# Performance work log

Measured on AMD Instinct MI355X. Metric: run time of the kernel, lower is better.

Reference implementation:

```python
import jax, jax.numpy as jnp
import numpy as np

T = 8192          # sequence length
D = 1024          # input_size
H = 16            # n_heads
HEAD = 64         # head_size = hidden_size // n_heads


def setup_inputs() -> dict:
    key = jax.random.key(0)
    ks = jax.random.split(key, 8)
    lim = (1.0 / HEAD) ** 0.5
    u = lambda k, shape: jax.random.uniform(k, shape, minval=-lim, maxval=lim, dtype=jnp.float32)
    return {
        "xs": jax.random.normal(ks[0], (T, D), dtype=jnp.float32),
        "if_weights": u(ks[1], (H, 2, D)),
        "o_weights": u(ks[2], (H, HEAD, D)),
        "kq_weights": u(ks[3], (H, 2 * HEAD, D)),
        "v_weights": u(ks[4], (H, HEAD, D)),
        "if_bias": u(ks[5], (H, 2)),
        "o_bias": u(ks[6], (H, HEAD)),
        "kvq_bias": u(ks[7], (H, 3, HEAD)),
    }


def reference(xs, if_weights, o_weights, kq_weights, v_weights, if_bias, o_bias, kvq_bias):
    inv_sqrt_head = 1.0 / jnp.sqrt(jnp.asarray(HEAD, jnp.float32))

    def step(state, x):
        h_prev, c_prev, m_prev, n_prev = state
        # gates
        i_f = jnp.einsum('htd,d->ht', if_weights, x) + if_bias          # (H, 2)
        o = jax.nn.sigmoid(jnp.einsum('hkd,d->hk', o_weights, x) + o_bias)  # (H, HEAD)
        i, f = i_f[:, 0], i_f[:, 1]
        # log-space stabilizer
        m = jnp.maximum(f + m_prev, i)
        i = jnp.exp(i - m)
        f = jnp.exp(f + m_prev - m)
        # key/query/value projections
        kq = jnp.einsum('hkd,d->hk', kq_weights, x)                      # (H, 2*HEAD)
        k, q = kq[:, :HEAD], kq[:, HEAD:]
        v = jnp.einsum('hkd,d->hk', v_weights, x)
        k = k * inv_sqrt_head + kvq_bias[:, 0]
        v = v + kvq_bias[:, 1]
        q = q + kvq_bias[:, 2]
        # state updates
        n = f[:, None] * n_prev + i[:, None] * k                          # (H, HEAD)
        c = f[:, None, None] * c_prev + i[:, None, None] * (v[:, :, None] * k[:, None, :])  # (H, HEAD, HEAD)
        # readout
        h = jnp.einsum('hij,hj->hi', c, q)                                # (H, HEAD)
        denom = jnp.maximum(jnp.abs(jnp.einsum('hj,hj->h', n, q)), 1.0)  # (H,)
        h = o * (h / denom[:, None])
        return (h, c, m, n), h.reshape(H * HEAD)

    init = (
        jnp.zeros((H, HEAD), jnp.float32),
        jnp.zeros((H, HEAD, HEAD), jnp.float32),
        jnp.zeros((H,), jnp.float32),
        jnp.zeros((H, HEAD), jnp.float32),
    )
    _, hs = jax.lax.scan(step, init, xs)
    return hs  # (T, hidden_size)
```

## Files before the change

### kernel.cpp

```cpp
#include <hip/hip_runtime.h>
#include <math.h>

#define T_LEN 8192
#define D_IN  1024
#define NH    16
#define NPAD  4224
#define NCH   128
#define NGRP  8
#define GSZ   16
#define NPACK 16896
#define NCONV 4096

typedef __attribute__((ext_vector_type(8))) _Float16 f16x8;
typedef __attribute__((ext_vector_type(4))) _Float16 f16x4;
typedef __attribute__((ext_vector_type(4))) float f32x4;

static const size_t OFF_WP   = 0;
static const size_t OFF_BG   = 2300000;
static const size_t OFF_BIAS = OFF_WP + (size_t)NPAD * D_IN;
static const size_t OFF_P    = OFF_BIAS + NPAD;
static const size_t OFF_M    = OFF_P + (size_t)T_LEN * NPAD;
static const size_t OFF_DC   = OFF_M + (size_t)T_LEN * NH;
static const size_t OFF_DN   = OFF_DC + (size_t)NCH * NH * 64 * 64;
static const size_t OFF_DL   = OFF_DN + (size_t)NCH * NH * 64;
static const size_t OFF_IF   = OFF_DL + (size_t)NCH * NH;

__device__ __forceinline__ void glds16(const void* g, void* l) {
  __builtin_amdgcn_global_load_lds(
      (const __attribute__((address_space(1))) void*)g,
      (__attribute__((address_space(3))) void*)l, 16, 0, 0);
}

__global__ __launch_bounds__(256) void pack_conv(
    const float* __restrict__ ifw, const float* __restrict__ ow,
    const float* __restrict__ kqw, const float* __restrict__ vw,
    const float* __restrict__ ifb, const float* __restrict__ ob,
    const float* __restrict__ kvqb, _Float16* __restrict__ Wph,
    float* __restrict__ bias,
    const float* __restrict__ X, _Float16* __restrict__ Xh) {
  int b = blockIdx.x;
  if (b < NPACK) {
    int idx = b * 256 + threadIdx.x;
    int n = idx >> 10, d = idx & 1023;
    float w = 0.f, bb = 0.f;
    if (n < 32) {
      int h = n >> 1, t = n & 1;
      w = ifw[(h * 2 + t) * D_IN + d];
      bb = ifb[h * 2 + t];
    } else if (n < 4128) {
      int r = n - 32;
      int h = r >> 8, j = r & 255;
      if (j < 64)       { w = kqw[(h * 128 + j) * D_IN + d] * 0.125f; bb = kvqb[(h * 3 + 0) * 64 + j]; }
      else if (j < 128) { w = kqw[(h * 128 + j) * D_IN + d];          bb = kvqb[(h * 3 + 2) * 64 + (j - 64)]; }
      else if (j < 192) { w = vw[(h * 64 + (j - 128)) * D_IN + d];    bb = kvqb[(h * 3 + 1) * 64 + (j - 128)]; }
      else              { w = ow[(h * 64 + (j - 192)) * D_IN + d];    bb = ob[h * 64 + (j - 192)]; }
    }
    Wph[(size_t)n * D_IN + d] = (_Float16)w;
    if (d == 0) bias[n] = bb;
  } else {
    int i = ((b - NPACK) * 256 + threadIdx.x) << 3;
    float4 v0 = *(const float4*)(X + i);
    float4 v1 = *(const float4*)(X + i + 4);
    f16x8 r;
    r[0] = (_Float16)v0.x; r[1] = (_Float16)v0.y; r[2] = (_Float16)v0.z; r[3] = (_Float16)v0.w;
    r[4] = (_Float16)v1.x; r[5] = (_Float16)v1.y; r[6] = (_Float16)v1.z; r[7] = (_Float16)v1.w;
    *(f16x8*)(Xh + i) = r;
  }
}

__global__ __launch_bounds__(256) void gemm_f16(
    const _Float16* __restrict__ Xh, const _Float16* __restrict__ Wph,
    const float* __restrict__ bias, _Float16* __restrict__ Ph) {
  __shared__ _Float16 As[2][128 * 32];
  __shared__ _Float16 Bs[2][128 * 32];
  int tid = threadIdx.x;
  int wave = tid >> 6, lane = tid & 63;
  int wgid = blockIdx.x;
  int virt = (wgid & 7) * 264 + (wgid >> 3);
  int mt = virt / 33, nt = virt % 33;
  int m0 = mt << 7, n0 = nt << 7;
  int wr = wave >> 1, wc = wave & 1;

  f32x4 acc[4][4];
  f32x4 zero = {0.f, 0.f, 0.f, 0.f};
#pragma unroll
  for (int i = 0; i < 4; ++i)
#pragma unroll
    for (int j = 0; j < 4; ++j) acc[i][j] = zero;

  int srow = lane >> 2;
  int scol = (((lane & 3) ^ ((lane >> 3) & 3)) << 3);
  const _Float16* ga = Xh + (size_t)(m0 + wave * 32 + srow) * D_IN + scol;
  const _Float16* gb = Wph + (size_t)(n0 + wave * 32 + srow) * D_IN + scol;
  int lds0 = (wave * 32) * 32;
  int lds1 = (wave * 32 + 16) * 32;

  int fr = lane & 15;
  int fko = (((lane >> 4) ^ ((fr >> 1) & 3)) << 3);

  glds16(ga, &As[0][lds0]);
  glds16(ga + 16 * D_IN, &As[0][lds1]);
  glds16(gb, &Bs[0][lds0]);
  glds16(gb + 16 * D_IN, &Bs[0][lds1]);
  __syncthreads();

  int cur = 0;
  for (int k0 = 0; k0 < D_IN; k0 += 32) {
    if (k0 + 32 < D_IN) {
      int kn = k0 + 32;
      glds16(ga + kn, &As[cur ^ 1][lds0]);
      glds16(ga + 16 * D_IN + kn, &As[cur ^ 1][lds1]);
      glds16(gb + kn, &Bs[cur ^ 1][lds0]);
      glds16(gb + 16 * D_IN + kn, &Bs[cur ^ 1][lds1]);
    }
    f16x8 a[4], b[4];
#pragma unroll
    for (int mi = 0; mi < 4; ++mi)
      a[mi] = *(const f16x8*)&As[cur][(wr * 64 + mi * 16 + fr) * 32 + fko];
#pragma unroll
    for (int ni = 0; ni < 4; ++ni)
      b[ni] = *(const f16x8*)&Bs[cur][(wc * 64 + ni * 16 + fr) * 32 + fko];
#pragma unroll
    for (int mi = 0; mi < 4; ++mi)
#pragma unroll
      for (int ni = 0; ni < 4; ++ni)
        acc[mi][ni] = __builtin_amdgcn_mfma_f32_16x16x32_f16(a[mi], b[ni], acc[mi][ni], 0, 0, 0);
    __syncthreads();
    cur ^= 1;
  }

  int cr = (lane >> 4) << 2;
  int cc = lane & 15;
#pragma unroll
  for (int mi = 0; mi < 4; ++mi) {
#pragma unroll
    for (int ni = 0; ni < 4; ++ni) {
      int col = n0 + wc * 64 + ni * 16 + cc;
      float bb = bias[col];
      size_t base = (size_t)(m0 + wr * 64 + mi * 16 + cr) * NPAD + col;
#pragma unroll
      for (int r = 0; r < 4; ++r)
        Ph[base + (size_t)r * NPAD] = (_Float16)(acc[mi][ni][r] + bb);
    }
  }
}

__global__ __launch_bounds__(256) void gemm_if(
    const float* __restrict__ X, const float* __restrict__ ifw,
    const float* __restrict__ ifb, float* __restrict__ IFc) {
  __shared__ float Xs[64 * 72];
  __shared__ float Ws[32 * 68];
  int tid = threadIdx.x;
  int r0 = blockIdx.x << 6;
  int nc = tid & 15;
  int rg = tid >> 4;
  int n0 = nc << 1;
  int sw = ((n0 >> 3) & 3) << 2;
  int sx = (rg & 3) << 2;

  float acc[4][2];
#pragma unroll
  for (int j = 0; j < 4; ++j) { acc[j][0] = 0.f; acc[j][1] = 0.f; }

  for (int k0 = 0; k0 < D_IN; k0 += 64) {
    __syncthreads();
#pragma unroll
    for (int i = 0; i < 4; ++i) {
      int fi = (i << 8) + tid;
      int row = fi >> 4, kk = (fi & 15) << 2;
      float4 v = *(const float4*)(X + (size_t)(r0 + row) * D_IN + k0 + kk);
      *(float4*)&Xs[row * 72 + (kk ^ (((row >> 2) & 3) << 2))] = v;
    }
#pragma unroll
    for (int i = 0; i < 2; ++i) {
      int fi = (i << 8) + tid;
      int row = fi >> 4, kk = (fi & 15) << 2;
      float4 v = *(const float4*)(ifw + (size_t)row * D_IN + k0 + kk);
      *(float4*)&Ws[row * 68 + (kk ^ (((row >> 3) & 3) << 2))] = v;
    }
    __syncthreads();
#pragma unroll
    for (int k4 = 0; k4 < 64; k4 += 4) {
      float4 w0 = *(const float4*)&Ws[n0 * 68 + (k4 ^ sw)];
      float4 w1 = *(const float4*)&Ws[(n0 + 1) * 68 + (k4 ^ sw)];
#pragma unroll
      for (int j = 0; j < 4; ++j) {
        float4 xv = *(const float4*)&Xs[((rg << 2) + j) * 72 + (k4 ^ sx)];
        acc[j][0] = fmaf(xv.x, w0.x, acc[j][0]);
        acc[j][0] = fmaf(xv.y, w0.y, acc[j][0]);
        acc[j][0] = fmaf(xv.z, w0.z, acc[j][0]);
        acc[j][0] = fmaf(xv.w, w0.w, acc[j][0]);
        acc[j][1] = fmaf(xv.x, w1.x, acc[j][1]);
        acc[j][1] = fmaf(xv.y, w1.y, acc[j][1]);
        acc[j][1] = fmaf(xv.z, w1.z, acc[j][1]);
        acc[j][1] = fmaf(xv.w, w1.w, acc[j][1]);
      }
    }
  }
  float b0 = ifb[n0], b1 = ifb[n0 + 1];
#pragma unroll
  for (int j = 0; j < 4; ++j) {
    int row = r0 + (rg << 2) + j;
    float2 st; st.x = acc[j][0] + b0; st.y = acc[j][1] + b1;
    *(float2*)(IFc + ((size_t)row << 5) + n0) = st;
  }
}

__global__ __launch_bounds__(256) void mscan(const float* __restrict__ IFc, float* __restrict__ M) {
  int h = blockIdx.x;
  int tid = threadIdx.x;
  int lane = tid & 63, wv = tid >> 6;
  int t0 = tid << 5;
  float F = 0.f, I = -1e30f;
#pragma unroll 8
  for (int u = 0; u < 32; ++u) {
    float2 v = *(const float2*)(IFc + ((size_t)(t0 + u) << 5) + (h << 1));
    I = fmaxf(I + v.y, v.x);
    F += v.y;
  }
#pragma unroll
  for (int d = 1; d < 64; d <<= 1) {
    float Fo = __shfl_up(F, d, 64);
    float Io = __shfl_up(I, d, 64);
    if (lane >= d) { I = fmaxf(Io + F, I); F = Fo + F; }
  }
  __shared__ float sF[4], sI[4];
  if (lane == 63) { sF[wv] = F; sI[wv] = I; }
  float Fe = __shfl_up(F, 1, 64);
  float Ie = __shfl_up(I, 1, 64);
  if (lane == 0) { Fe = 0.f; Ie = -1e30f; }
  __syncthreads();
  float Fp = 0.f, Ip = -1e30f;
  for (int w = 0; w < wv; ++w) { Ip = fmaxf(Ip + sF[w], sI[w]); Fp += sF[w]; }
  float Ft = Fp + Fe;
  float It = fmaxf(Ip + Fe, Ie);
  float m = fmaxf(Ft, It);
#pragma unroll 8
  for (int u = 0; u < 32; ++u) {
    float2 v = *(const float2*)(IFc + ((size_t)(t0 + u) << 5) + (h << 1));
    m = fmaxf(v.y + m, v.x);
    M[(size_t)(t0 + u) * NH + h] = m;
  }
}

__global__ __launch_bounds__(256) void d1_dc(
    const _Float16* __restrict__ Ph, const float* __restrict__ IFc,
    const float* __restrict__ M,
    _Float16* __restrict__ DCh, float* __restrict__ DN, float* __restrict__ DL) {
  int c = blockIdx.x >> 4, h = blockIdx.x & 15;
  int t0 = c << 6, hb = 32 + (h << 8);
  int tid = threadIdx.x;
  int lane = tid & 63, wave = tid >> 6;
  __shared__ _Float16 Kt[64 * 72];
  __shared__ _Float16 Vt[64 * 72];
  __shared__ float gl[64];
#pragma unroll
  for (int i = 0; i < 2; ++i) {
    int fq = (i << 8) + tid;
    int s = fq >> 3, b8 = (fq & 7) << 3;
    const _Float16* row = Ph + (size_t)(t0 + s) * NPAD + hb;
    f16x8 kv = *(const f16x8*)(row + b8);
    f16x8 vv = *(const f16x8*)(row + 128 + b8);
#pragma unroll
    for (int j = 0; j < 8; ++j) {
      Kt[(b8 + j) * 72 + s] = kv[j];
      Vt[(b8 + j) * 72 + s] = vv[j];
    }
  }
  if (tid < 64) {
    float2 iff = *(const float2*)(IFc + ((size_t)(t0 + tid) << 5) + (h << 1));
    float iv = iff.x, fv = iff.y;
    float cs = fv;
#pragma unroll
    for (int dd = 1; dd < 64; dd <<= 1) {
      float o = __shfl_up(cs, dd, 64);
      cs += (tid >= dd) ? o : 0.f;
    }
    float cumL = __shfl(cs, 63, 64);
    float mL = M[(size_t)(t0 + 63) * NH + h];
    gl[tid] = __expf(cumL - cs + iv - mL);
    if (tid == 0) {
      float mstart = (c > 0) ? M[(size_t)(t0 - 1) * NH + h] : 0.f;
      DL[(c << 4) + h] = __expf(mstart + cumL - mL);
    }
  }
  __syncthreads();
  if (tid < 64) {
    float acc = 0.f;
#pragma unroll
    for (int s = 0; s < 64; ++s) acc = fmaf(gl[s], (float)Kt[tid * 72 + s], acc);
    DN[((size_t)(c << 4) + h) * 64 + tid] = acc;
  }
  int arow = lane & 15;
  int kq = (lane >> 4) << 3;
  int aR = (wave << 4) + arow;
  f16x8 ag0, ag1;
#pragma unroll
  for (int j = 0; j < 8; ++j) {
    ag0[j] = (_Float16)(gl[kq + j] * (float)Vt[aR * 72 + kq + j]);
    ag1[j] = (_Float16)(gl[32 + kq + j] * (float)Vt[aR * 72 + 32 + kq + j]);
  }
  f32x4 accD[4];
  f32x4 zero = {0.f, 0.f, 0.f, 0.f};
#pragma unroll
  for (int n = 0; n < 4; ++n) accD[n] = zero;
#pragma unroll
  for (int n = 0; n < 4; ++n) {
    f16x8 b0 = *(const f16x8*)&Kt[((n << 4) + arow) * 72 + kq];
    f16x8 b1 = *(const f16x8*)&Kt[((n << 4) + arow) * 72 + 32 + kq];
    accD[n] = __builtin_amdgcn_mfma_f32_16x16x32_f16(ag0, b0, accD[n], 0, 0, 0);
    accD[n] = __builtin_amdgcn_mfma_f32_16x16x32_f16(ag1, b1, accD[n], 0, 0, 0);
  }
  __syncthreads();
  int crow = (lane >> 4) << 2, cc = lane & 15;
#pragma unroll
  for (int n = 0; n < 4; ++n)
#pragma unroll
    for (int r = 0; r < 4; ++r)
      Vt[((wave << 4) + crow + r) * 72 + (n << 4) + cc] = (_Float16)accD[n][r];
  __syncthreads();
  size_t base = ((size_t)(c << 4) + h) << 12;
#pragma unroll
  for (int i = 0; i < 2; ++i) {
    int fq = (i << 8) + tid;
    int a = fq >> 3, b8 = (fq & 7) << 3;
    *(f16x8*)(DCh + base + ((size_t)a << 6) + b8) = *(const f16x8*)&Vt[a * 72 + b8];
  }
}

__global__ __launch_bounds__(256) void d2a(
    const _Float16* __restrict__ DCh, const float* __restrict__ DN,
    const float* __restrict__ DL,
    float* __restrict__ BgDC, float* __restrict__ BgDN, float* __restrict__ Ag) {
  int bid = blockIdx.x, tid = threadIdx.x;
  if (bid < 2048) {
    int linear = (bid << 8) + tid;
    int g = linear >> 16, e = linear & 65535;
    int h = e >> 12;
    float carry = 0.f, a = 1.f;
    size_t idx = (size_t)e + ((size_t)g << 4) * 65536;
    float v = (float)DCh[idx];
    for (int u = 0; u < GSZ; ++u) {
      float dl = DL[(((g << 4) + u) << 4) + h];
      float vn = (u < GSZ - 1) ? (float)DCh[idx + 65536] : 0.f;
      carry = fmaf(dl, carry, v);
      a *= dl;
      v = vn;
      idx += 65536;
    }
    BgDC[((size_t)g << 16) + e] = carry;
    if ((e & 4095) == 0) Ag[(g << 4) + h] = a;
  } else {
    int linear = ((bid - 2048) << 8) + tid;
    int g = linear >> 10, e = linear & 1023;
    int h = e >> 6;
    float carry = 0.f;
    size_t idx = (size_t)e + ((size_t)g << 4) * 1024;
    float v = DN[idx];
    for (int u = 0; u < GSZ; ++u) {
      float dl = DL[(((g << 4) + u) << 4) + h];
      float vn = (u < GSZ - 1) ? DN[idx + 1024] : 0.f;
      carry = fmaf(dl, carry, v);
      v = vn;
      idx += 1024;
    }
    BgDN[(g << 10) + e] = carry;
  }
}

__global__ __launch_bounds__(256) void d2c(
    _Float16* __restrict__ DCh, float* __restrict__ DN,
    const float* __restrict__ DL,
    const float* __restrict__ BgDC, const float* __restrict__ BgDN,
    const float* __restrict__ Ag) {
  int bid = blockIdx.x, tid = threadIdx.x;
  if (bid < 2048) {
    int linear = (bid << 8) + tid;
    int g = linear >> 16, e = linear & 65535;
    int h = e >> 12;
    float P = 0.f;
    for (int gp = 0; gp < g; ++gp)
      P = fmaf(Ag[(gp << 4) + h], P, BgDC[((size_t)gp << 16) + e]);
    float carry = P;
    size_t idx = (size_t)e + ((size_t)g << 4) * 65536;
    float v = (float)DCh[idx];
    for (int u = 0; u < GSZ; ++u) {
      float dl = DL[(((g << 4) + u) << 4) + h];
      float vn = (u < GSZ - 1) ? (float)DCh[idx + 65536] : 0.f;
      DCh[idx] = (_Float16)carry;
      carry = fmaf(dl, carry, v);
      v = vn;
      idx += 65536;
    }
  } else {
    int linear = ((bid - 2048) << 8) + tid;
    int g = linear >> 10, e = linear & 1023;
    int h = e >> 6;
    float P = 0.f;
    for (int gp = 0; gp < g; ++gp)
      P = fmaf(Ag[(gp << 4) + h], P, BgDN[(gp << 10) + e]);
    float carry = P;
    size_t idx = (size_t)e + ((size_t)g << 4) * 1024;
    float v = DN[idx];
    for (int u = 0; u < GSZ; ++u) {
      float dl = DL[(((g << 4) + u) << 4) + h];
      float vn = (u < GSZ - 1) ? DN[idx + 1024] : 0.f;
      DN[idx] = carry;
      carry = fmaf(dl, carry, v);
      v = vn;
      idx += 1024;
    }
  }
}

__global__ __launch_bounds__(256) void d3_out(
    const _Float16* __restrict__ Ph, const float* __restrict__ IFc,
    const float* __restrict__ M,
    const _Float16* __restrict__ CS, const float* __restrict__ NS,
    float* __restrict__ out) {
  int c = blockIdx.x >> 4, h = blockIdx.x & 15;
  int t0 = c << 6, hb = 32 + (h << 8);
  int tid = threadIdx.x;
  int lane = tid & 63, wave = tid >> 6;
  __shared__ _Float16 Kh[64 * 72];
  __shared__ _Float16 Qh[64 * 72];
  __shared__ _Float16 Vt[64 * 72];
  __shared__ _Float16 Ch[64 * 72];
  __shared__ _Float16 Oh[64 * 72];
  __shared__ _Float16 Pl[64 * 72];
  __shared__ float cf[64], il[64], ml[64], dl[64], nq[64], nsl[64];

#pragma unroll
  for (int i = 0; i < 2; ++i) {
    int fq = (i << 8) + tid;
    int s = fq >> 3, b8 = (fq & 7) << 3;
    const _Float16* row = Ph + (size_t)(t0 + s) * NPAD + hb;
    f16x8 kv = *(const f16x8*)(row + b8);
    f16x8 qv = *(const f16x8*)(row + 64 + b8);
    f16x8 vv = *(const f16x8*)(row + 128 + b8);
    f16x8 ov = *(const f16x8*)(row + 192 + b8);
    f16x8 cv = *(const f16x8*)(CS + ((((size_t)(c << 4)) + h) << 12) + ((size_t)s << 6) + b8);
    *(f16x8*)&Kh[s * 72 + b8] = kv;
    *(f16x8*)&Qh[s * 72 + b8] = qv;
    *(f16x8*)&Oh[s * 72 + b8] = ov;
    *(f16x8*)&Ch[s * 72 + b8] = cv;
#pragma unroll
    for (int j = 0; j < 8; ++j) Vt[(b8 + j) * 72 + s] = vv[j];
  }
  __syncthreads();

  float iv = 0.f, mt = 0.f, cs = 0.f;
  if (tid < 64) {
    float2 iff = *(const float2*)(IFc + ((size_t)(t0 + tid) << 5) + (h << 1));
    iv = iff.x;
    float fv = iff.y;
    mt = M[(size_t)(t0 + tid) * NH + h];
    nsl[tid] = NS[((size_t)(c << 4) + h) * 64 + tid];
    cs = fv;
#pragma unroll
    for (int dd = 1; dd < 64; dd <<= 1) {
      float o = __shfl_up(cs, dd, 64);
      cs += (tid >= dd) ? o : 0.f;
    }
  }
  __syncthreads();
  if (tid < 64) {
    cf[tid] = cs; il[tid] = iv; ml[tid] = mt;
    float mstart = (c > 0) ? M[(size_t)(t0 - 1) * NH + h] : 0.f;
    dl[tid] = __expf(mstart + cs - mt);
    float acc = 0.f;
#pragma unroll
    for (int b = 0; b < 64; ++b) acc = fmaf(nsl[b], (float)Qh[tid * 72 + b], acc);
    nq[tid] = acc;
  }
  __syncthreads();

  int band = wave << 4;
  int arow = lane & 15;
  int kq = (lane >> 4) << 3;
  int crow = (lane >> 4) << 2;

  f16x8 aq0 = *(const f16x8*)&Qh[(band + arow) * 72 + kq];
  f16x8 aq1 = *(const f16x8*)&Qh[(band + arow) * 72 + 32 + kq];

  f32x4 S[4];
  f32x4 zero = {0.f, 0.f, 0.f, 0.f};
#pragma unroll
  for (int n = 0; n < 4; ++n) S[n] = zero;
#pragma unroll
  for (int n = 0; n < 4; ++n) {
    f16x8 b0 = *(const f16x8*)&Kh[((n << 4) + arow) * 72 + kq];
    f16x8 b1 = *(const f16x8*)&Kh[((n << 4) + arow) * 72 + 32 + kq];
    S[n] = __builtin_amdgcn_mfma_f32_16x16x32_f16(aq0, b0, S[n], 0, 0, 0);
    S[n] = __builtin_amdgcn_mfma_f32_16x16x32_f16(aq1, b1, S[n], 0, 0, 0);
  }

  float cft[4], mlt[4];
#pragma unroll
  for (int r = 0; r < 4; ++r) {
    int t = band + crow + r;
    cft[r] = cf[t]; mlt[r] = ml[t];
  }
  float rsum[4] = {0.f, 0.f, 0.f, 0.f};
#pragma unroll
  for (int n = 0; n < 4; ++n) {
    int s = (n << 4) + arow;
    float cfs = cf[s], ils = il[s];
#pragma unroll
    for (int r = 0; r < 4; ++r) {
      int t = band + crow + r;
      float w = (s <= t) ? __expf(cft[r] - cfs + ils - mlt[r]) : 0.f;
      float p = S[n][r] * w;
      rsum[r] += p;
      Pl[t * 72 + s] = (_Float16)p;
    }
  }
#pragma unroll
  for (int r = 0; r < 4; ++r) {
    float p = rsum[r];
    p += __shfl_xor(p, 1);
    p += __shfl_xor(p, 2);
    p += __shfl_xor(p, 4);
    p += __shfl_xor(p, 8);
    rsum[r] = p;
  }
  __syncthreads();

  f16x8 ap0 = *(const f16x8*)&Pl[(band + arow) * 72 + kq];
  f16x8 ap1 = *(const f16x8*)&Pl[(band + arow) * 72 + 32 + kq];
  f32x4 H[4], I[4];
#pragma unroll
  for (int n = 0; n < 4; ++n) { H[n] = zero; I[n] = zero; }
#pragma unroll
  for (int n = 0; n < 4; ++n) {
    f16x8 bv0 = *(const f16x8*)&Vt[((n << 4) + arow) * 72 + kq];
    f16x8 bv1 = *(const f16x8*)&Vt[((n << 4) + arow) * 72 + 32 + kq];
    H[n] = __builtin_amdgcn_mfma_f32_16x16x32_f16(ap0, bv0, H[n], 0, 0, 0);
    H[n] = __builtin_amdgcn_mfma_f32_16x16x32_f16(ap1, bv1, H[n], 0, 0, 0);
    f16x8 bc0 = *(const f16x8*)&Ch[((n << 4) + arow) * 72 + kq];
    f16x8 bc1 = *(const f16x8*)&Ch[((n << 4) + arow) * 72 + 32 + kq];
    I[n] = __builtin_amdgcn_mfma_f32_16x16x32_f16(aq0, bc0, I[n], 0, 0, 0);
    I[n] = __builtin_amdgcn_mfma_f32_16x16x32_f16(aq1, bc1, I[n], 0, 0, 0);
  }

#pragma unroll
  for (int r = 0; r < 4; ++r) {
    int t = band + crow + r;
    float dt = dl[t];
    float dn = fmaf(dt, nq[t], rsum[r]);
    float rinv = 1.f / fmaxf(fabsf(dn), 1.f);
    float* orow = out + (size_t)(t0 + t) * 1024 + (h << 6);
#pragma unroll
    for (int n = 0; n < 4; ++n) {
      int a = (n << 4) + arow;
      float o = 1.f / (1.f + __expf(-(float)Oh[t * 72 + a]));
      orow[a] = o * (fmaf(dt, I[n][r], H[n][r]) * rinv);
    }
  }
}

extern "C" void kernel_launch(void* const* d_in, const int* in_sizes, int n_in,
                              void* d_out, int out_size, void* d_ws, size_t ws_size,
                              hipStream_t stream) {
  const float* xs   = (const float*)d_in[0];
  const float* ifw  = (const float*)d_in[1];
  const float* ow   = (const float*)d_in[2];
  const float* kqw  = (const float*)d_in[3];
  const float* vw   = (const float*)d_in[4];
  const float* ifb  = (const float*)d_in[5];
  const float* ob   = (const float*)d_in[6];
  const float* kvqb = (const float*)d_in[7];
  float* ws   = (float*)d_ws;
  _Float16* Wph = (_Float16*)(ws + OFF_WP);
  float* BgDC = ws + OFF_BG;
  float* BgDN = BgDC + (size_t)NGRP * 65536;
  float* Ag   = BgDN + (size_t)NGRP * 1024;
  float* bias = ws + OFF_BIAS;
  _Float16* Phm = (_Float16*)(ws + OFF_P);
  float* Mm   = ws + OFF_M;
  _Float16* DCh = (_Float16*)(ws + OFF_DC);
  _Float16* Xh  = (_Float16*)(ws + OFF_DC);
  float* DN   = ws + OFF_DN;
  float* DL   = ws + OFF_DL;
  float* IFc  = ws + OFF_IF;
  float* outp = (float*)d_out;

  hipLaunchKernelGGL(pack_conv, dim3(NPACK + NCONV), dim3(256), 0, stream,
                     ifw, ow, kqw, vw, ifb, ob, kvqb, Wph, bias, xs, Xh);
  hipLaunchKernelGGL(gemm_f16, dim3(33 * 64), dim3(256), 0, stream,
                     Xh, Wph, bias, Phm);
  hipLaunchKernelGGL(gemm_if, dim3(T_LEN / 64), dim3(256), 0, stream, xs, ifw, ifb, IFc);
  hipLaunchKernelGGL(mscan, dim3(NH), dim3(256), 0, stream, IFc, Mm);
  hipLaunchKernelGGL(d1_dc, dim3(NCH * NH), dim3(256), 0, stream, Phm, IFc, Mm, DCh, DN, DL);
  hipLaunchKernelGGL(d2a, dim3(2080), dim3(256), 0, stream, DCh, DN, DL, BgDC, BgDN, Ag);
  hipLaunchKernelGGL(d2c, dim3(2080), dim3(256), 0, stream, DCh, DN, DL, BgDC, BgDN, Ag);
  hipLaunchKernelGGL(d3_out, dim3(NCH * NH), dim3(256), 0, stream, Phm, IFc, Mm, DCh, DN, outp);
}
```

Baseline: 224.2 us.

## Triple-buffer f16 GEMM with manual waitcnt pipelining and halve gemm_if row tile

```diff
diff --git a/kernel.cpp b/kernel.cpp
--- a/kernel.cpp
+++ b/kernel.cpp
@@ -71,8 +71,8 @@
 __global__ __launch_bounds__(256) void gemm_f16(
     const _Float16* __restrict__ Xh, const _Float16* __restrict__ Wph,
     const float* __restrict__ bias, _Float16* __restrict__ Ph) {
-  __shared__ _Float16 As[2][128 * 32];
-  __shared__ _Float16 Bs[2][128 * 32];
+  __shared__ _Float16 As[3][128 * 32];
+  __shared__ _Float16 Bs[3][128 * 32];
   int tid = threadIdx.x;
   int wave = tid >> 6, lane = tid & 63;
   int wgid = blockIdx.x;
@@ -98,36 +98,43 @@
   int fr = lane & 15;
   int fko = (((lane >> 4) ^ ((fr >> 1) & 3)) << 3);
 
-  glds16(ga, &As[0][lds0]);
-  glds16(ga + 16 * D_IN, &As[0][lds1]);
-  glds16(gb, &Bs[0][lds0]);
-  glds16(gb + 16 * D_IN, &Bs[0][lds1]);
-  __syncthreads();
-
-  int cur = 0;
-  for (int k0 = 0; k0 < D_IN; k0 += 32) {
-    if (k0 + 32 < D_IN) {
-      int kn = k0 + 32;
-      glds16(ga + kn, &As[cur ^ 1][lds0]);
-      glds16(ga + 16 * D_IN + kn, &As[cur ^ 1][lds1]);
-      glds16(gb + kn, &Bs[cur ^ 1][lds0]);
-      glds16(gb + 16 * D_IN + kn, &Bs[cur ^ 1][lds1]);
+#define STG(T, S) do { int ko_ = (T) << 5;                         \
+    glds16(ga + ko_, &As[S][lds0]);                                \
+    glds16(ga + 16 * D_IN + ko_, &As[S][lds1]);                    \
+    glds16(gb + ko_, &Bs[S][lds0]);                                \
+    glds16(gb + 16 * D_IN + ko_, &Bs[S][lds1]);                    \
+  } while (0)
+
+  STG(0, 0);
+  STG(1, 1);
+
+  int slot = 0;
+  for (int i = 0; i < 32; ++i) {
+    if (i < 31) asm volatile("s_waitcnt vmcnt(4)" ::: "memory");
+    else        asm volatile("s_waitcnt vmcnt(0)" ::: "memory");
+    __builtin_amdgcn_s_barrier();
+    __builtin_amdgcn_sched_barrier(0);
+    if (i < 30) {
+      int ns = slot + 2; if (ns >= 3) ns -= 3;
+      STG(i + 2, ns);
     }
     f16x8 a[4], b[4];
 #pragma unroll
     for (int mi = 0; mi < 4; ++mi)
-      a[mi] = *(const f16x8*)&As[cur][(wr * 64 + mi * 16 + fr) * 32 + fko];
+      a[mi] = *(const f16x8*)&As[slot][(wr * 64 + mi * 16 + fr) * 32 + fko];
 #pragma unroll
     for (int ni = 0; ni < 4; ++ni)
-      b[ni] = *(const f16x8*)&Bs[cur][(wc * 64 + ni * 16 + fr) * 32 + fko];
+      b[ni] = *(const f16x8*)&Bs[slot][(wc * 64 + ni * 16 + fr) * 32 + fko];
+    __builtin_amdgcn_s_setprio(1);
 #pragma unroll
     for (int mi = 0; mi < 4; ++mi)
 #pragma unroll
       for (int ni = 0; ni < 4; ++ni)
         acc[mi][ni] = __builtin_amdgcn_mfma_f32_16x16x32_f16(a[mi], b[ni], acc[mi][ni], 0, 0, 0);
-    __syncthreads();
-    cur ^= 1;
-  }
+    __builtin_amdgcn_s_setprio(0);
+    slot = slot + 1; if (slot >= 3) slot = 0;
+  }
+#undef STG
 
   int cr = (lane >> 4) << 2;
   int cc = lane & 15;
@@ -148,24 +155,23 @@
 __global__ __launch_bounds__(256) void gemm_if(
     const float* __restrict__ X, const float* __restrict__ ifw,
     const float* __restrict__ ifb, float* __restrict__ IFc) {
-  __shared__ float Xs[64 * 72];
+  __shared__ float Xs[32 * 72];
   __shared__ float Ws[32 * 68];
   int tid = threadIdx.x;
-  int r0 = blockIdx.x << 6;
+  int r0 = blockIdx.x << 5;
   int nc = tid & 15;
   int rg = tid >> 4;
   int n0 = nc << 1;
   int sw = ((n0 >> 3) & 3) << 2;
-  int sx = (rg & 3) << 2;
-
-  float acc[4][2];
-#pragma unroll
-  for (int j = 0; j < 4; ++j) { acc[j][0] = 0.f; acc[j][1] = 0.f; }
+  int sx = ((rg >> 1) & 3) << 2;
+
+  float acc[2][2];
+  acc[0][0] = acc[0][1] = acc[1][0] = acc[1][1] = 0.f;
 
   for (int k0 = 0; k0 < D_IN; k0 += 64) {
     __syncthreads();
 #pragma unroll
-    for (int i = 0; i < 4; ++i) {
+    for (int i = 0; i < 2; ++i) {
       int fi = (i << 8) + tid;
       int row = fi >> 4, kk = (fi & 15) << 2;
       float4 v = *(const float4*)(X + (size_t)(r0 + row) * D_IN + k0 + kk);
@@ -184,8 +190,8 @@
       float4 w0 = *(const float4*)&Ws[n0 * 68 + (k4 ^ sw)];
       float4 w1 = *(const float4*)&Ws[(n0 + 1) * 68 + (k4 ^ sw)];
 #pragma unroll
-      for (int j = 0; j < 4; ++j) {
-        float4 xv = *(const float4*)&Xs[((rg << 2) + j) * 72 + (k4 ^ sx)];
+      for (int j = 0; j < 2; ++j) {
+        float4 xv = *(const float4*)&Xs[((rg << 1) + j) * 72 + (k4 ^ sx)];
         acc[j][0] = fmaf(xv.x, w0.x, acc[j][0]);
         acc[j][0] = fmaf(xv.y, w0.y, acc[j][0]);
         acc[j][0] = fmaf(xv.z, w0.z, acc[j][0]);
@@ -199,8 +205,8 @@
   }
   float b0 = ifb[n0], b1 = ifb[n0 + 1];
 #pragma unroll
-  for (int j = 0; j < 4; ++j) {
-    int row = r0 + (rg << 2) + j;
+  for (int j = 0; j < 2; ++j) {
+    int row = r0 + (rg << 1) + j;
     float2 st; st.x = acc[j][0] + b0; st.y = acc[j][1] + b1;
     *(float2*)(IFc + ((size_t)row << 5) + n0) = st;
   }
@@ -589,7 +595,7 @@
                      ifw, ow, kqw, vw, ifb, ob, kvqb, Wph, bias, xs, Xh);
   hipLaunchKernelGGL(gemm_f16, dim3(33 * 64), dim3(256), 0, stream,
                      Xh, Wph, bias, Phm);
-  hipLaunchKernelGGL(gemm_if, dim3(T_LEN / 64), dim3(256), 0, stream, xs, ifw, ifb, IFc);
+  hipLaunchKernelGGL(gemm_if, dim3(T_LEN / 32), dim3(256), 0, stream, xs, ifw, ifb, IFc);
   hipLaunchKernelGGL(mscan, dim3(NH), dim3(256), 0, stream, IFc, Mm);
   hipLaunchKernelGGL(d1_dc, dim3(NCH * NH), dim3(256), 0, stream, Phm, IFc, Mm, DCh, DN, DL);
   hipLaunchKernelGGL(d2a, dim3(2080), dim3(256), 0, stream, DCh, DN, DL, BgDC, BgDN, Ag);
```

Result: faster. 215.6 us (-3.8%).
